# Optimization experiments

Hardware: AMD Instinct MI355X
Metric: run time of the kernel (lower is better)

Reference implementation:

```python
import jax, jax.numpy as jnp
import numpy as np

# Adaptive softmax config (PyTorch AdaptiveLogSoftmaxWithLoss defaults, div_value=4)
N_CLASSES = 50000
CUTOFFS = (2000, 10000)          # shortlist size 2000; clusters [2000,10000), [10000,50000)
SHORTLIST = CUTOFFS[0]
HEAD_SIZE = SHORTLIST + 2        # shortlist + one logit per cluster
IN_FEAT = 512                    # output_size of MLP == in_features of adaptive softmax
HSZ0, HSZ1 = 128, 32             # in_features // 4**(i+1)
C0 = CUTOFFS[1] - CUTOFFS[0]     # 8000
C1 = N_CLASSES - CUTOFFS[1]      # 40000


def setup_inputs() -> dict:
    key = jax.random.key(0)
    ks = jax.random.split(key, 16)
    s = 0.02
    inp = {
        "x": jax.random.normal(ks[0], (4096, 512), jnp.float32),
        "t": jax.random.randint(ks[1], (4096,), 0, N_CLASSES, jnp.int64),
        # MLP params: 512 -> 2048 -> 128 -> 512, ReLU after each
        "W1": jax.random.normal(ks[2], (2048, 512), jnp.float32) * s,
        "b1": jnp.zeros((2048,), jnp.float32),
        "W2": jax.random.normal(ks[3], (128, 2048), jnp.float32) * s,
        "b2": jnp.zeros((128,), jnp.float32),
        "W3": jax.random.normal(ks[4], (512, 128), jnp.float32) * s,
        "b3": jnp.zeros((512,), jnp.float32),
        # adaptive softmax head: shortlist + 2 cluster logits
        "head_W": jax.random.normal(ks[5], (HEAD_SIZE, IN_FEAT), jnp.float32) * s,
        "head_b": jnp.zeros((HEAD_SIZE,), jnp.float32),
        # tail cluster 0: 512 -> 128 -> 8000 (no bias, no activation)
        "t0a": jax.random.normal(ks[6], (HSZ0, IN_FEAT), jnp.float32) * s,
        "t0b": jax.random.normal(ks[7], (C0, HSZ0), jnp.float32) * s,
        # tail cluster 1: 512 -> 32 -> 40000
        "t1a": jax.random.normal(ks[8], (HSZ1, IN_FEAT), jnp.float32) * s,
        "t1b": jax.random.normal(ks[9], (C1, HSZ1), jnp.float32) * s,
    }
    return inp


def _mlp(x, W1, b1, W2, b2, W3, b3):
    h = jax.nn.relu(x @ W1.T + b1)
    h = jax.nn.relu(h @ W2.T + b2)
    return jax.nn.relu(h @ W3.T + b3)   # [N, 512]


def _adaptive_log_softmax(score, t, head_W, head_b, t0a, t0b, t1a, t1b):
    n = score.shape[0]
    rows = jnp.arange(n)
    head_lsm = jax.nn.log_softmax(score @ head_W.T + head_b, axis=-1)   # [N, 2002]
    # tail clusters: two low-rank projections then log-softmax over cluster classes
    tail0_lsm = jax.nn.log_softmax((score @ t0a.T) @ t0b.T, axis=-1)    # [N, 8000]
    tail1_lsm = jax.nn.log_softmax((score @ t1a.T) @ t1b.T, axis=-1)    # [N, 40000]

    lp_short = head_lsm[rows, jnp.clip(t, 0, SHORTLIST - 1)]
    lp_c0 = head_lsm[:, SHORTLIST] + tail0_lsm[rows, jnp.clip(t - CUTOFFS[0], 0, C0 - 1)]
    lp_c1 = head_lsm[:, SHORTLIST + 1] + tail1_lsm[rows, jnp.clip(t - CUTOFFS[1], 0, C1 - 1)]

    out = jnp.where(t < CUTOFFS[0], lp_short, jnp.where(t < CUTOFFS[1], lp_c0, lp_c1))  # [N]
    loss = -jnp.mean(out)
    return out, loss


def reference(x, t, W1, b1, W2, b2, W3, b3, head_W, head_b, t0a, t0b, t1a, t1b):
    score = _mlp(x, W1, b1, W2, b2, W3, b3)
    out, loss = _adaptive_log_softmax(score, t, head_W, head_b, t0a, t0b, t1a, t1b)
    return out, loss
```

## Files before the change

kernel.cpp:

```cpp
#include <hip/hip_runtime.h>
#include <math.h>

typedef __attribute__((ext_vector_type(8))) short bf16x8;
typedef __attribute__((ext_vector_type(4))) float f32x4;

#define NROWS 4096
#define SHORTLIST 2000
#define HEADC 2002
#define CUT1 10000
#define C0_CLS 8000
#define C1_CLS 40000
#define L2E 1.4426950408889634f
#define LN2 0.6931471805599453f

#define NH_P  16
#define NC0_P 25
#define NC1_P 125

__device__ __forceinline__ float fexp2(float x) {
#if __has_builtin(__builtin_amdgcn_exp2f)
  return __builtin_amdgcn_exp2f(x);
#else
  return exp2f(x);
#endif
}

__device__ __forceinline__ unsigned short f2b(float f) {
  unsigned u = __float_as_uint(f);
  unsigned r = (u + 0x7FFFu + ((u >> 16) & 1u)) >> 16;
  return (unsigned short)r;
}
__device__ __forceinline__ float b2f(unsigned short u) {
  return __uint_as_float(((unsigned)u) << 16);
}

__global__ __launch_bounds__(256) void cvt_all(
    const float* __restrict__ s0, unsigned short* __restrict__ d0,
    const float* __restrict__ s1, unsigned short* __restrict__ d1,
    const float* __restrict__ s2, unsigned short* __restrict__ d2,
    const float* __restrict__ s3, unsigned short* __restrict__ d3,
    const float* __restrict__ s4, unsigned short* __restrict__ d4,
    const float* __restrict__ s5, unsigned short* __restrict__ d5,
    const float* __restrict__ s6, unsigned short* __restrict__ d6,
    const float* __restrict__ s7, unsigned short* __restrict__ d7,
    const float* __restrict__ s8, unsigned short* __restrict__ d8)
{
  const float* src; unsigned short* dst; int n4;
  switch (blockIdx.y) {
    case 0: src = s0; dst = d0; n4 = 4096 * 512 / 4;   break;
    case 1: src = s1; dst = d1; n4 = 2048 * 512 / 4;   break;
    case 2: src = s2; dst = d2; n4 = 128 * 2048 / 4;   break;
    case 3: src = s3; dst = d3; n4 = 512 * 128 / 4;    break;
    case 4: src = s4; dst = d4; n4 = HEADC * 512 / 4;  break;
    case 5: src = s5; dst = d5; n4 = 128 * 512 / 4;    break;
    case 6: src = s6; dst = d6; n4 = 8000 * 128 / 4;   break;
    case 7: src = s7; dst = d7; n4 = 32 * 512 / 4;     break;
    default: src = s8; dst = d8; n4 = 40000 * 32 / 4;  break;
  }
  for (int i = blockIdx.x * 256 + threadIdx.x; i < n4; i += 256 * gridDim.x) {
    float4 v = ((const float4*)src)[i];
    ushort4 o;
    o.x = f2b(v.x); o.y = f2b(v.y); o.z = f2b(v.z); o.w = f2b(v.w);
    ((ushort4*)dst)[i] = o;
  }
}

template<bool BIAS, bool RELU, bool F32OUT>
__global__ __launch_bounds__(256) void gemm_lds(
    const unsigned short* __restrict__ A, const unsigned short* __restrict__ W,
    const float* __restrict__ bias, void* __restrict__ outp,
    int M, int N, int lda, int Kseg)
{
  __shared__ __align__(16) unsigned short As[128 * 32];
  __shared__ __align__(16) unsigned short Bs[128 * 32];

  const int tid  = threadIdx.x;
  const int lane = tid & 63;
  const int wv   = tid >> 6;
  const int cl   = lane & 15;
  const int ko   = lane >> 4;
  const int wr   = (wv >> 1) * 64;
  const int wc   = (wv & 1) * 64;
  const int row0 = blockIdx.y * 128;
  const int col0 = blockIdx.x * 128;
  const int koff = blockIdx.z * Kseg;

  const int sr0 = tid >> 2;
  const int ssl = tid & 3;

  f32x4 acc[4][4];
#pragma unroll
  for (int p = 0; p < 4; ++p)
#pragma unroll
    for (int q = 0; q < 4; ++q) acc[p][q] = (f32x4){0.f, 0.f, 0.f, 0.f};

  const unsigned short* aSrc = A + (size_t)(row0 + sr0) * lda + koff + ssl * 8;
  const unsigned short* bSrc = W + (size_t)(col0 + sr0) * lda + koff + ssl * 8;
  const size_t half = (size_t)64 * lda;

  bf16x8 sa0 = *(const bf16x8*)(aSrc);
  bf16x8 sa1 = *(const bf16x8*)(aSrc + half);
  bf16x8 sb0 = *(const bf16x8*)(bSrc);
  bf16x8 sb1 = *(const bf16x8*)(bSrc + half);

  const int nK = Kseg / 32;
  for (int ks = 0; ks < nK; ++ks) {
    __syncthreads();
    *(bf16x8*)&As[(size_t)sr0 * 32 + ssl * 8]        = sa0;
    *(bf16x8*)&As[(size_t)(sr0 + 64) * 32 + ssl * 8] = sa1;
    *(bf16x8*)&Bs[(size_t)sr0 * 32 + ssl * 8]        = sb0;
    *(bf16x8*)&Bs[(size_t)(sr0 + 64) * 32 + ssl * 8] = sb1;
    __syncthreads();
    if (ks + 1 < nK) {
      const int k1 = (ks + 1) * 32;
      sa0 = *(const bf16x8*)(aSrc + k1);
      sa1 = *(const bf16x8*)(aSrc + k1 + half);
      sb0 = *(const bf16x8*)(bSrc + k1);
      sb1 = *(const bf16x8*)(bSrc + k1 + half);
    }
    bf16x8 aF[4], bF[4];
#pragma unroll
    for (int p = 0; p < 4; ++p)
      aF[p] = *(const bf16x8*)&As[(size_t)(wr + p * 16 + cl) * 32 + ko * 8];
#pragma unroll
    for (int q = 0; q < 4; ++q)
      bF[q] = *(const bf16x8*)&Bs[(size_t)(wc + q * 16 + cl) * 32 + ko * 8];
#pragma unroll
    for (int p = 0; p < 4; ++p)
#pragma unroll
      for (int q = 0; q < 4; ++q)
        acc[p][q] = __builtin_amdgcn_mfma_f32_16x16x32_bf16(aF[p], bF[q], acc[p][q], 0, 0, 0);
  }

  if constexpr (F32OUT) {
    float* P = (float*)outp + (size_t)blockIdx.z * M * N;
#pragma unroll
    for (int q = 0; q < 4; ++q) {
      const int col = col0 + wc + q * 16 + cl;
#pragma unroll
      for (int p = 0; p < 4; ++p)
#pragma unroll
        for (int j = 0; j < 4; ++j) {
          const int R = row0 + wr + p * 16 + 4 * ko + j;
          P[(size_t)R * N + col] = acc[p][q][j];
        }
    }
  } else {
    unsigned short* C = (unsigned short*)outp;
#pragma unroll
    for (int q = 0; q < 4; ++q) {
      const int col = col0 + wc + q * 16 + cl;
      float bs = 0.f;
      if (BIAS) bs = bias[col];
#pragma unroll
      for (int p = 0; p < 4; ++p)
#pragma unroll
        for (int j = 0; j < 4; ++j) {
          const int R = row0 + wr + p * 16 + 4 * ko + j;
          float v = acc[p][q][j] + bs;
          if (RELU) v = fmaxf(v, 0.f);
          C[(size_t)R * N + col] = f2b(v);
        }
    }
  }
}

template<int SK, bool BIAS, bool RELU>
__global__ __launch_bounds__(256) void splitk_reduce(
    const float* __restrict__ P, const float* __restrict__ bias,
    unsigned short* __restrict__ out, int MN4, int N)
{
  const int i = blockIdx.x * 256 + threadIdx.x;
  if (i >= MN4) return;
  float4 v = ((const float4*)P)[i];
#pragma unroll
  for (int z = 1; z < SK; ++z) {
    float4 p = ((const float4*)(P + (size_t)z * MN4 * 4))[i];
    v.x += p.x; v.y += p.y; v.z += p.z; v.w += p.w;
  }
  if (BIAS) {
    const int col = (i % (N / 4)) * 4;
    float4 b = *(const float4*)(bias + col);
    v.x += b.x; v.y += b.y; v.z += b.z; v.w += b.w;
  }
  if (RELU) {
    v.x = fmaxf(v.x, 0.f); v.y = fmaxf(v.y, 0.f);
    v.z = fmaxf(v.z, 0.f); v.w = fmaxf(v.w, 0.f);
  }
  ushort4 o;
  o.x = f2b(v.x); o.y = f2b(v.y); o.z = f2b(v.z); o.w = f2b(v.w);
  ((ushort4*)out)[i] = o;
}

__global__ __launch_bounds__(256) void head_gemm_lse(
    const unsigned short* __restrict__ A,
    const unsigned short* __restrict__ W,
    const float* __restrict__ bias,
    float* __restrict__ pm, float* __restrict__ ps)
{
  __shared__ __align__(16) unsigned short As[128 * 32];
  __shared__ __align__(16) unsigned short Bs[128 * 32];
  __shared__ float lm[4][64], ls[4][64];

  const int lda  = 512;
  const int tid  = threadIdx.x;
  const int lane = tid & 63;
  const int wv   = tid >> 6;
  const int cl   = lane & 15;
  const int ko   = lane >> 4;
  const int wr   = (wv >> 1) * 64;
  const int wc   = (wv & 1) * 64;
  const int row0 = blockIdx.y * 128;
  const int col0 = blockIdx.x * 128;

  const int sr0 = tid >> 2;
  const int ssl = tid & 3;

  f32x4 acc[4][4];
#pragma unroll
  for (int p = 0; p < 4; ++p)
#pragma unroll
    for (int q = 0; q < 4; ++q) acc[p][q] = (f32x4){0.f, 0.f, 0.f, 0.f};

  const unsigned short* aSrc = A + (size_t)(row0 + sr0) * lda + ssl * 8;
  const unsigned short* bSrc0 = W + (size_t)min(col0 + sr0, HEADC - 1) * lda + ssl * 8;
  const unsigned short* bSrc1 = W + (size_t)min(col0 + sr0 + 64, HEADC - 1) * lda + ssl * 8;
  const size_t half = (size_t)64 * lda;

  bf16x8 sa0 = *(const bf16x8*)(aSrc);
  bf16x8 sa1 = *(const bf16x8*)(aSrc + half);
  bf16x8 sb0 = *(const bf16x8*)(bSrc0);
  bf16x8 sb1 = *(const bf16x8*)(bSrc1);

  const int nK = 512 / 32;
  for (int ks = 0; ks < nK; ++ks) {
    __syncthreads();
    *(bf16x8*)&As[(size_t)sr0 * 32 + ssl * 8]        = sa0;
    *(bf16x8*)&As[(size_t)(sr0 + 64) * 32 + ssl * 8] = sa1;
    *(bf16x8*)&Bs[(size_t)sr0 * 32 + ssl * 8]        = sb0;
    *(bf16x8*)&Bs[(size_t)(sr0 + 64) * 32 + ssl * 8] = sb1;
    __syncthreads();
    if (ks + 1 < nK) {
      const int k1 = (ks + 1) * 32;
      sa0 = *(const bf16x8*)(aSrc + k1);
      sa1 = *(const bf16x8*)(aSrc + k1 + half);
      sb0 = *(const bf16x8*)(bSrc0 + k1);
      sb1 = *(const bf16x8*)(bSrc1 + k1);
    }
    bf16x8 aF[4], bF[4];
#pragma unroll
    for (int p = 0; p < 4; ++p)
      aF[p] = *(const bf16x8*)&As[(size_t)(wr + p * 16 + cl) * 32 + ko * 8];
#pragma unroll
    for (int q = 0; q < 4; ++q)
      bF[q] = *(const bf16x8*)&Bs[(size_t)(wc + q * 16 + cl) * 32 + ko * 8];
#pragma unroll
    for (int p = 0; p < 4; ++p)
#pragma unroll
      for (int q = 0; q < 4; ++q)
        acc[p][q] = __builtin_amdgcn_mfma_f32_16x16x32_bf16(aF[p], bF[q], acc[p][q], 0, 0, 0);
  }

  float bl2[4]; int colq[4];
#pragma unroll
  for (int q = 0; q < 4; ++q) {
    colq[q] = col0 + wc + q * 16 + cl;
    bl2[q] = bias[min(colq[q], HEADC - 1)] * L2E;
  }

  float mr[4][4], sr_[4][4];
#pragma unroll
  for (int p = 0; p < 4; ++p)
#pragma unroll
    for (int j = 0; j < 4; ++j) {
      float vv[4], mm = -3e38f;
#pragma unroll
      for (int q = 0; q < 4; ++q) {
        float v = fmaf(acc[p][q][j], L2E, bl2[q]);
        if (colq[q] >= HEADC) v = -1e30f;
        vv[q] = v;
        mm = fmaxf(mm, v);
      }
      float ss = 0.f;
#pragma unroll
      for (int q = 0; q < 4; ++q) ss += fexp2(vv[q] - mm);
      mr[p][j] = mm;
      sr_[p][j] = ss;
    }

#pragma unroll
  for (int mask = 1; mask <= 8; mask <<= 1) {
#pragma unroll
    for (int p = 0; p < 4; ++p)
#pragma unroll
      for (int j = 0; j < 4; ++j) {
        const float mo = __shfl_xor(mr[p][j], mask);
        const float so = __shfl_xor(sr_[p][j], mask);
        const float mn = fmaxf(mr[p][j], mo);
        sr_[p][j] = sr_[p][j] * fexp2(mr[p][j] - mn) + so * fexp2(mo - mn);
        mr[p][j] = mn;
      }
  }

  if (cl == 0) {
#pragma unroll
    for (int p = 0; p < 4; ++p)
#pragma unroll
      for (int j = 0; j < 4; ++j) {
        lm[wv][p * 16 + 4 * ko + j] = mr[p][j];
        ls[wv][p * 16 + 4 * ko + j] = sr_[p][j];
      }
  }
  __syncthreads();
  if (tid < 128) {
    const int pair = tid >> 6, idx = tid & 63;
    const float m0 = lm[pair * 2][idx], m1 = lm[pair * 2 + 1][idx];
    const float M = fmaxf(m0, m1);
    const float S = ls[pair * 2][idx] * fexp2(m0 - M) + ls[pair * 2 + 1][idx] * fexp2(m1 - M);
    const int grow = row0 + tid;
    pm[(size_t)blockIdx.x * NROWS + grow] = M;
    ps[(size_t)blockIdx.x * NROWS + grow] = S;
  }
}

template<int WR, int WC, bool BIAS, bool RELU>
__global__ __launch_bounds__(256) void gemm_mfma(
    const unsigned short* __restrict__ A, const unsigned short* __restrict__ W,
    const float* __restrict__ bias, unsigned short* __restrict__ C,
    int M, int N, int K)
{
  const int lane = threadIdx.x & 63;
  const int wv   = threadIdx.x >> 6;
  const int cl   = lane & 15;
  const int ko   = lane >> 4;
  const int rw   = (blockIdx.y * WR + (wv / WC)) * 64;
  const int cw   = (blockIdx.x * WC + (wv % WC)) * 32;

  f32x4 acc[4][2];
#pragma unroll
  for (int p = 0; p < 4; ++p)
#pragma unroll
    for (int q = 0; q < 2; ++q) acc[p][q] = (f32x4){0.f, 0.f, 0.f, 0.f};

  const unsigned short* ap = A + (size_t)(rw + cl) * K + ko * 8;
  const unsigned short* bp = W + (size_t)(cw + cl) * K + ko * 8;
  const size_t rstep = (size_t)16 * K;

#pragma unroll 2
  for (int kb = 0; kb < K; kb += 32) {
    bf16x8 a[4], b[2];
#pragma unroll
    for (int p = 0; p < 4; ++p) a[p] = *(const bf16x8*)(ap + p * rstep + kb);
#pragma unroll
    for (int q = 0; q < 2; ++q) b[q] = *(const bf16x8*)(bp + q * rstep + kb);
#pragma unroll
    for (int p = 0; p < 4; ++p)
#pragma unroll
      for (int q = 0; q < 2; ++q)
        acc[p][q] = __builtin_amdgcn_mfma_f32_16x16x32_bf16(a[p], b[q], acc[p][q], 0, 0, 0);
  }

#pragma unroll
  for (int q = 0; q < 2; ++q) {
    const int col = cw + q * 16 + cl;
    if (col >= N) continue;
    float bs = 0.f;
    if (BIAS) bs = bias[col];
#pragma unroll
    for (int p = 0; p < 4; ++p) {
#pragma unroll
      for (int j = 0; j < 4; ++j) {
        const int R = rw + p * 16 + 4 * ko + j;
        float v = acc[p][q][j] + bs;
        if (RELU) v = fmaxf(v, 0.f);
        C[(size_t)R * N + col] = f2b(v);
      }
    }
  }
}

template<int KBLK, int ROWT, int U, int NIT>
__global__ __launch_bounds__(256) void fused_lse_tail(
    const unsigned short* __restrict__ H,
    const unsigned short* __restrict__ W,
    int NCB,
    float* __restrict__ pm, float* __restrict__ ps)
{
  const int K    = KBLK * 32;
  const int lane = threadIdx.x & 63;
  const int wv   = threadIdx.x >> 6;
  const int cl   = lane & 15;
  const int ko   = lane >> 4;
  const int r0   = blockIdx.x * (64 * ROWT) + wv * (16 * ROWT);

  bf16x8 aF[ROWT][KBLK];
#pragma unroll
  for (int rt = 0; rt < ROWT; ++rt) {
    const unsigned short* ap = H + (size_t)(r0 + rt * 16 + cl) * K + ko * 8;
#pragma unroll
    for (int kk = 0; kk < KBLK; ++kk) aF[rt][kk] = *(const bf16x8*)(ap + kk * 32);
  }

  float m[ROWT][4], s[ROWT][4];
#pragma unroll
  for (int rt = 0; rt < ROWT; ++rt)
#pragma unroll
    for (int j = 0; j < 4; ++j) { m[rt][j] = -1e30f; s[rt][j] = 0.f; }

  const unsigned short* wbase =
      W + (size_t)(blockIdx.y * (U * NIT) * 16 + cl) * K + ko * 8;
  const size_t chunkstep = (size_t)16 * K;

  bf16x8 bA[U][KBLK], bB[U][KBLK];

  auto loadB = [&](bf16x8 (&bf)[U][KBLK], int it) {
    const unsigned short* p = wbase + (size_t)it * U * chunkstep;
#pragma unroll
    for (int u = 0; u < U; ++u)
#pragma unroll
      for (int kk = 0; kk < KBLK; ++kk)
        bf[u][kk] = *(const bf16x8*)(p + u * chunkstep + kk * 32);
  };

  auto consume = [&](bf16x8 (&bf)[U][KBLK]) {
    f32x4 acc[ROWT][U];
#pragma unroll
    for (int rt = 0; rt < ROWT; ++rt)
#pragma unroll
      for (int u = 0; u < U; ++u) acc[rt][u] = (f32x4){0.f, 0.f, 0.f, 0.f};
#pragma unroll
    for (int kk = 0; kk < KBLK; ++kk)
#pragma unroll
      for (int u = 0; u < U; ++u)
#pragma unroll
        for (int rt = 0; rt < ROWT; ++rt)
          acc[rt][u] = __builtin_amdgcn_mfma_f32_16x16x32_bf16(aF[rt][kk], bf[u][kk], acc[rt][u], 0, 0, 0);

    float nm[ROWT][4];
#pragma unroll
    for (int rt = 0; rt < ROWT; ++rt)
#pragma unroll
      for (int j = 0; j < 4; ++j) nm[rt][j] = m[rt][j];
#pragma unroll
    for (int rt = 0; rt < ROWT; ++rt)
#pragma unroll
      for (int u = 0; u < U; ++u)
#pragma unroll
        for (int j = 0; j < 4; ++j)
          nm[rt][j] = fmaxf(nm[rt][j], acc[rt][u][j] * L2E);

    float dd = -3e38f;
#pragma unroll
    for (int rt = 0; rt < ROWT; ++rt)
#pragma unroll
      for (int j = 0; j < 4; ++j) dd = fmaxf(dd, nm[rt][j] - m[rt][j]);

    if (__any(dd > 8.f)) {
#pragma unroll
      for (int rt = 0; rt < ROWT; ++rt)
#pragma unroll
        for (int j = 0; j < 4; ++j) {
          s[rt][j] *= fexp2(m[rt][j] - nm[rt][j]);
          m[rt][j] = nm[rt][j];
        }
    }
#pragma unroll
    for (int rt = 0; rt < ROWT; ++rt)
#pragma unroll
      for (int u = 0; u < U; ++u)
#pragma unroll
        for (int j = 0; j < 4; ++j)
          s[rt][j] += fexp2(fmaf(acc[rt][u][j], L2E, -m[rt][j]));
  };

  loadB(bA, 0);
#pragma unroll
  for (int it = 0; it < NIT; it += 2) {
    loadB(bB, it + 1);
    consume(bA);
    if (it + 2 < NIT) loadB(bA, it + 2);
    consume(bB);
  }

#pragma unroll
  for (int mask = 1; mask <= 8; mask <<= 1) {
#pragma unroll
    for (int rt = 0; rt < ROWT; ++rt)
#pragma unroll
      for (int j = 0; j < 4; ++j) {
        const float mo = __shfl_xor(m[rt][j], mask);
        const float so = __shfl_xor(s[rt][j], mask);
        const float mn = fmaxf(m[rt][j], mo);
        s[rt][j] = s[rt][j] * fexp2(m[rt][j] - mn) + so * fexp2(mo - mn);
        m[rt][j] = mn;
      }
  }
  if (cl == 0) {
#pragma unroll
    for (int rt = 0; rt < ROWT; ++rt)
#pragma unroll
      for (int j = 0; j < 4; ++j) {
        const int R = r0 + rt * 16 + 4 * ko + j;
        pm[(size_t)blockIdx.y * NROWS + R] = m[rt][j];
        ps[(size_t)blockIdx.y * NROWS + R] = s[rt][j];
      }
  }
}

__global__ __launch_bounds__(256) void gather_kernel(
    const unsigned short* __restrict__ Sb,
    const unsigned short* __restrict__ hWb,
    const float* __restrict__ head_b,
    const unsigned short* __restrict__ h0b,
    const unsigned short* __restrict__ t0bb,
    const unsigned short* __restrict__ h1b,
    const unsigned short* __restrict__ t1bb,
    const int* __restrict__ t,
    float* __restrict__ gsh, float* __restrict__ gc0, float* __restrict__ gc1,
    float* __restrict__ tg0, float* __restrict__ tg1)
{
  const int lane = threadIdx.x & 63;
  const int row  = blockIdx.x * 4 + (threadIdx.x >> 6);
  const int tv   = t[row];
  const int ch   = min(max(tv, 0), SHORTLIST - 1);
  const int c0   = min(max(tv - SHORTLIST, 0), C0_CLS - 1);
  const int c1   = min(max(tv - CUT1, 0), C1_CLS - 1);

  float acc[5] = {0.f, 0.f, 0.f, 0.f, 0.f};

  {
    bf16x8 sv = *(const bf16x8*)(Sb + (size_t)row * 512 + lane * 8);
    bf16x8 w0 = *(const bf16x8*)(hWb + (size_t)ch * 512 + lane * 8);
    bf16x8 w1 = *(const bf16x8*)(hWb + (size_t)SHORTLIST * 512 + lane * 8);
    bf16x8 w2 = *(const bf16x8*)(hWb + (size_t)(SHORTLIST + 1) * 512 + lane * 8);
#pragma unroll
    for (int e = 0; e < 8; ++e) {
      const float sf = b2f((unsigned short)sv[e]);
      acc[0] = fmaf(sf, b2f((unsigned short)w0[e]), acc[0]);
      acc[1] = fmaf(sf, b2f((unsigned short)w1[e]), acc[1]);
      acc[2] = fmaf(sf, b2f((unsigned short)w2[e]), acc[2]);
    }
  }
  if (lane < 16) {
    bf16x8 hv = *(const bf16x8*)(h0b + (size_t)row * 128 + lane * 8);
    bf16x8 wv = *(const bf16x8*)(t0bb + (size_t)c0 * 128 + lane * 8);
#pragma unroll
    for (int e = 0; e < 8; ++e)
      acc[3] = fmaf(b2f((unsigned short)hv[e]), b2f((unsigned short)wv[e]), acc[3]);
  }
  if (lane < 4) {
    bf16x8 hv = *(const bf16x8*)(h1b + (size_t)row * 32 + lane * 8);
    bf16x8 wv = *(const bf16x8*)(t1bb + (size_t)c1 * 32 + lane * 8);
#pragma unroll
    for (int e = 0; e < 8; ++e)
      acc[4] = fmaf(b2f((unsigned short)hv[e]), b2f((unsigned short)wv[e]), acc[4]);
  }

#pragma unroll
  for (int mask = 1; mask < 64; mask <<= 1)
#pragma unroll
    for (int k = 0; k < 5; ++k) acc[k] += __shfl_xor(acc[k], mask);

  if (lane == 0) {
    gsh[row] = acc[0] + head_b[ch];
    gc0[row] = acc[1] + head_b[SHORTLIST];
    gc1[row] = acc[2] + head_b[SHORTLIST + 1];
    tg0[row] = acc[3];
    tg1[row] = acc[4];
  }
}

__global__ __launch_bounds__(256) void combine_kernel(
    const int* __restrict__ t,
    const float* __restrict__ pmh, const float* __restrict__ psh,
    const float* __restrict__ gsh, const float* __restrict__ gc0,
    const float* __restrict__ gc1,
    const float* __restrict__ pm0, const float* __restrict__ ps0,
    const float* __restrict__ tg0,
    const float* __restrict__ pm1, const float* __restrict__ ps1,
    const float* __restrict__ tg1,
    float* __restrict__ out)
{
  const int r = blockIdx.x * 256 + threadIdx.x;
  if (r >= NROWS) return;

  float M = -1e30f, S = 0.f;
  for (int c = 0; c < NH_P; ++c) M = fmaxf(M, pmh[c * NROWS + r]);
  for (int c = 0; c < NH_P; ++c) S += psh[c * NROWS + r] * fexp2(pmh[c * NROWS + r] - M);
  const float hl = (M + log2f(S)) * LN2;

  const int tv = t[r];
  float o;
  if (tv < SHORTLIST) {
    o = gsh[r] - hl;
  } else if (tv < CUT1) {
    float M0 = -1e30f, S0 = 0.f;
    for (int c = 0; c < NC0_P; ++c) M0 = fmaxf(M0, pm0[c * NROWS + r]);
    for (int c = 0; c < NC0_P; ++c) S0 += ps0[c * NROWS + r] * fexp2(pm0[c * NROWS + r] - M0);
    o = (gc0[r] - hl) + (tg0[r] - (M0 + log2f(S0)) * LN2);
  } else {
    float M1 = -1e30f, S1 = 0.f;
    for (int c = 0; c < NC1_P; ++c) M1 = fmaxf(M1, pm1[c * NROWS + r]);
    for (int c = 0; c < NC1_P; ++c) S1 += ps1[c * NROWS + r] * fexp2(pm1[c * NROWS + r] - M1);
    o = (gc1[r] - hl) + (tg1[r] - (M1 + log2f(S1)) * LN2);
  }
  out[r] = o;
}

__global__ __launch_bounds__(256) void loss_kernel(
    const float* __restrict__ out, float* __restrict__ loss)
{
  __shared__ float sred[256];
  const int tid = threadIdx.x;
  float s = 0.f;
  for (int i = tid; i < NROWS; i += 256) s += out[i];
  sred[tid] = s;
  __syncthreads();
  for (int st = 128; st > 0; st >>= 1) {
    if (tid < st) sred[tid] += sred[tid + st];
    __syncthreads();
  }
  if (tid == 0) *loss = -sred[0] / (float)NROWS;
}

extern "C" void kernel_launch(void* const* d_in, const int* in_sizes, int n_in,
                              void* d_out, int out_size, void* d_ws, size_t ws_size,
                              hipStream_t stream)
{
  const float* x      = (const float*)d_in[0];
  const int*   t      = (const int*)  d_in[1];
  const float* W1     = (const float*)d_in[2];
  const float* b1     = (const float*)d_in[3];
  const float* W2     = (const float*)d_in[4];
  const float* b2     = (const float*)d_in[5];
  const float* W3     = (const float*)d_in[6];
  const float* b3     = (const float*)d_in[7];
  const float* head_W = (const float*)d_in[8];
  const float* head_b = (const float*)d_in[9];
  const float* t0a    = (const float*)d_in[10];
  const float* t0b    = (const float*)d_in[11];
  const float* t1a    = (const float*)d_in[12];
  const float* t1b    = (const float*)d_in[13];

  unsigned short* p16 = (unsigned short*)d_ws;
  unsigned short* xb  = p16; p16 += 4096ull * 512;
  unsigned short* W1b = p16; p16 += 2048ull * 512;
  unsigned short* W2b = p16; p16 += 128ull  * 2048;
  unsigned short* W3b = p16; p16 += 512ull  * 128;
  unsigned short* hWb = p16; p16 += (size_t)HEADC * 512;
  unsigned short* t0ab= p16; p16 += 128ull  * 512;
  unsigned short* t0bb= p16; p16 += 8000ull * 128;
  unsigned short* t1ab= p16; p16 += 32ull   * 512;
  unsigned short* t1bb= p16; p16 += 40000ull* 32;
  unsigned short* H1b = p16; p16 += 4096ull * 2048;
  unsigned short* H2b = p16; p16 += 4096ull * 128;
  unsigned short* Sb  = p16; p16 += 4096ull * 512;
  unsigned short* h0b = p16; p16 += 4096ull * 128;
  unsigned short* h1b = p16; p16 += 4096ull * 32;

  float* pf  = (float*)p16;
  float* pmh = pf; pf += 4096 * NH_P;
  float* psh = pf; pf += 4096 * NH_P;
  float* pm0 = pf; pf += 4096 * NC0_P;
  float* ps0 = pf; pf += 4096 * NC0_P;
  float* pm1 = pf; pf += 4096 * NC1_P;
  float* ps1 = pf; pf += 4096 * NC1_P;
  float* gsh = pf; pf += 4096;
  float* gc0 = pf; pf += 4096;
  float* gc1 = pf; pf += 4096;
  float* tg0 = pf; pf += 4096;
  float* tg1 = pf; pf += 4096;
  float* Pbuf = pf; pf += 4ull * 4096 * 128;

  float* out = (float*)d_out;

  const dim3 blk(256);

  cvt_all<<<dim3(256, 9), blk, 0, stream>>>(
      x, xb, W1, W1b, W2, W2b, W3, W3b, head_W, hWb,
      t0a, t0ab, t0b, t0bb, t1a, t1ab, t1b, t1bb);

  gemm_lds<true, true, false><<<dim3(16, 32), blk, 0, stream>>>(
      xb, W1b, b1, H1b, 4096, 2048, 512, 512);
  gemm_lds<false, false, true><<<dim3(1, 32, 4), blk, 0, stream>>>(
      H1b, W2b, nullptr, Pbuf, 4096, 128, 2048, 512);
  splitk_reduce<4, true, true><<<dim3(512), blk, 0, stream>>>(
      Pbuf, b2, H2b, 4096 * 128 / 4, 128);
  gemm_lds<true, true, false><<<dim3(4, 32), blk, 0, stream>>>(
      H2b, W3b, b3, Sb, 4096, 512, 128, 128);

  gemm_lds<false, false, true><<<dim3(1, 32, 4), blk, 0, stream>>>(
      Sb, t0ab, nullptr, Pbuf, 4096, 128, 512, 128);
  splitk_reduce<4, false, false><<<dim3(512), blk, 0, stream>>>(
      Pbuf, nullptr, h0b, 4096 * 128 / 4, 128);
  gemm_mfma<4, 1, false, false><<<dim3(1, 16), blk, 0, stream>>>(
      Sb, t1ab, nullptr, h1b, 4096, 32, 512);

  head_gemm_lse<<<dim3(16, 32), blk, 0, stream>>>(Sb, hWb, head_b, pmh, psh);

  fused_lse_tail<4, 2, 2, 10><<<dim3(32, NC0_P), blk, 0, stream>>>(h0b, t0bb, NC0_P, pm0, ps0);
  fused_lse_tail<1, 2, 5, 4 ><<<dim3(32, NC1_P), blk, 0, stream>>>(h1b, t1bb, NC1_P, pm1, ps1);

  gather_kernel<<<dim3(NROWS / 4), blk, 0, stream>>>(
      Sb, hWb, head_b, h0b, t0bb, h1b, t1bb, t, gsh, gc0, gc1, tg0, tg1);

  combine_kernel<<<dim3((NROWS + 255) / 256), blk, 0, stream>>>(
      t, pmh, psh, gsh, gc0, gc1, pm0, ps0, tg0, pm1, ps1, tg1, out);
  loss_kernel<<<dim3(1), blk, 0, stream>>>(out, out + NROWS);
}
```

Before: 301.1 us.

## Pre-scale score by log2e, swizzle blocks across XCDs, split tail exp accumulators

The final MLP layer now multiplies its output by log2(e) before rounding to bf16. All downstream logits are therefore already in base-2 units, which removes the per-element L2E multiply in the head and tail LSE kernels. Head bias in the gather step and the final ln2 conversion in the combine step are adjusted to match. GEMM and head kernels also remap block indices so neighbouring tiles land on the same XCD for L2 reuse, and the tail LSE splits its exp sum into two accumulators to shorten the dependency chain. Rescaling before the bf16 rounding slightly changes the numerics.

```diff
diff --git a/kernel.cpp b/kernel.cpp
--- a/kernel.cpp
+++ b/kernel.cpp
@@ -32,6 +32,15 @@
 }
 __device__ __forceinline__ float b2f(unsigned short u) {
   return __uint_as_float(((unsigned)u) << 16);
+}
+
+__device__ __forceinline__ void xcd_swz(int& bx, int& by) {
+  const int gx = gridDim.x;
+  const int nwg = gx * gridDim.y;
+  const int orig = by * gx + bx;
+  const int wg = (orig & 7) * (nwg >> 3) + (orig >> 3);
+  bx = wg % gx;
+  by = wg / gx;
 }
 
 __global__ __launch_bounds__(256) void cvt_all(
@@ -65,7 +74,7 @@
   }
 }
 
-template<bool BIAS, bool RELU, bool F32OUT>
+template<bool BIAS, bool RELU, bool F32OUT, bool SCL>
 __global__ __launch_bounds__(256) void gemm_lds(
     const unsigned short* __restrict__ A, const unsigned short* __restrict__ W,
     const float* __restrict__ bias, void* __restrict__ outp,
@@ -73,6 +82,9 @@
 {
   __shared__ __align__(16) unsigned short As[128 * 32];
   __shared__ __align__(16) unsigned short Bs[128 * 32];
+
+  int bx = blockIdx.x, by = blockIdx.y;
+  xcd_swz(bx, by);
 
   const int tid  = threadIdx.x;
   const int lane = tid & 63;
@@ -81,8 +93,8 @@
   const int ko   = lane >> 4;
   const int wr   = (wv >> 1) * 64;
   const int wc   = (wv & 1) * 64;
-  const int row0 = blockIdx.y * 128;
-  const int col0 = blockIdx.x * 128;
+  const int row0 = by * 128;
+  const int col0 = bx * 128;
   const int koff = blockIdx.z * Kseg;
 
   const int sr0 = tid >> 2;
@@ -159,6 +171,7 @@
           const int R = row0 + wr + p * 16 + 4 * ko + j;
           float v = acc[p][q][j] + bs;
           if (RELU) v = fmaxf(v, 0.f);
+          if (SCL)  v *= L2E;
           C[(size_t)R * N + col] = f2b(v);
         }
     }
@@ -201,6 +214,9 @@
   __shared__ __align__(16) unsigned short As[128 * 32];
   __shared__ __align__(16) unsigned short Bs[128 * 32];
   __shared__ float lm[4][64], ls[4][64];
+
+  int bx = blockIdx.x, by = blockIdx.y;
+  xcd_swz(bx, by);
 
   const int lda  = 512;
   const int tid  = threadIdx.x;
@@ -210,8 +226,8 @@
   const int ko   = lane >> 4;
   const int wr   = (wv >> 1) * 64;
   const int wc   = (wv & 1) * 64;
-  const int row0 = blockIdx.y * 128;
-  const int col0 = blockIdx.x * 128;
+  const int row0 = by * 128;
+  const int col0 = bx * 128;
 
   const int sr0 = tid >> 2;
   const int ssl = tid & 3;
@@ -273,14 +289,14 @@
   for (int p = 0; p < 4; ++p)
 #pragma unroll
     for (int j = 0; j < 4; ++j) {
-      float vv[4], mm = -3e38f;
+      float vv[4];
 #pragma unroll
       for (int q = 0; q < 4; ++q) {
-        float v = fmaf(acc[p][q][j], L2E, bl2[q]);
+        float v = acc[p][q][j] + bl2[q];
         if (colq[q] >= HEADC) v = -1e30f;
         vv[q] = v;
-        mm = fmaxf(mm, v);
       }
+      const float mm = fmaxf(fmaxf(vv[0], vv[1]), fmaxf(vv[2], vv[3]));
       float ss = 0.f;
 #pragma unroll
       for (int q = 0; q < 4; ++q) ss += fexp2(vv[q] - mm);
@@ -318,8 +334,8 @@
     const float M = fmaxf(m0, m1);
     const float S = ls[pair * 2][idx] * fexp2(m0 - M) + ls[pair * 2 + 1][idx] * fexp2(m1 - M);
     const int grow = row0 + tid;
-    pm[(size_t)blockIdx.x * NROWS + grow] = M;
-    ps[(size_t)blockIdx.x * NROWS + grow] = S;
+    pm[(size_t)bx * NROWS + grow] = M;
+    ps[(size_t)bx * NROWS + grow] = S;
   }
 }
 
@@ -401,11 +417,11 @@
     for (int kk = 0; kk < KBLK; ++kk) aF[rt][kk] = *(const bf16x8*)(ap + kk * 32);
   }
 
-  float m[ROWT][4], s[ROWT][4];
+  float m[ROWT][4], s[ROWT][4], s2[ROWT][4];
 #pragma unroll
   for (int rt = 0; rt < ROWT; ++rt)
 #pragma unroll
-    for (int j = 0; j < 4; ++j) { m[rt][j] = -1e30f; s[rt][j] = 0.f; }
+    for (int j = 0; j < 4; ++j) { m[rt][j] = -1e30f; s[rt][j] = 0.f; s2[rt][j] = 0.f; }
 
   const unsigned short* wbase =
       W + (size_t)(blockIdx.y * (U * NIT) * 16 + cl) * K + ko * 8;
@@ -436,32 +452,32 @@
         for (int rt = 0; rt < ROWT; ++rt)
           acc[rt][u] = __builtin_amdgcn_mfma_f32_16x16x32_bf16(aF[rt][kk], bf[u][kk], acc[rt][u], 0, 0, 0);
 
-    float nm[ROWT][4];
+    float cm[ROWT][4];
 #pragma unroll
     for (int rt = 0; rt < ROWT; ++rt)
 #pragma unroll
-      for (int j = 0; j < 4; ++j) nm[rt][j] = m[rt][j];
+      for (int j = 0; j < 4; ++j) {
+        float c = acc[rt][0][j];
+#pragma unroll
+        for (int u = 1; u < U; ++u) c = fmaxf(c, acc[rt][u][j]);
+        cm[rt][j] = c;
+      }
+
+    float dd = -3e38f;
 #pragma unroll
     for (int rt = 0; rt < ROWT; ++rt)
 #pragma unroll
-      for (int u = 0; u < U; ++u)
-#pragma unroll
-        for (int j = 0; j < 4; ++j)
-          nm[rt][j] = fmaxf(nm[rt][j], acc[rt][u][j] * L2E);
-
-    float dd = -3e38f;
-#pragma unroll
-    for (int rt = 0; rt < ROWT; ++rt)
-#pragma unroll
-      for (int j = 0; j < 4; ++j) dd = fmaxf(dd, nm[rt][j] - m[rt][j]);
+      for (int j = 0; j < 4; ++j) dd = fmaxf(dd, cm[rt][j] - m[rt][j]);
 
     if (__any(dd > 8.f)) {
 #pragma unroll
       for (int rt = 0; rt < ROWT; ++rt)
 #pragma unroll
         for (int j = 0; j < 4; ++j) {
-          s[rt][j] *= fexp2(m[rt][j] - nm[rt][j]);
-          m[rt][j] = nm[rt][j];
+          const float mn = fmaxf(m[rt][j], cm[rt][j]);
+          const float sc = fexp2(m[rt][j] - mn);
+          s[rt][j] *= sc; s2[rt][j] *= sc;
+          m[rt][j] = mn;
         }
     }
 #pragma unroll
@@ -469,8 +485,10 @@
 #pragma unroll
       for (int u = 0; u < U; ++u)
 #pragma unroll
-        for (int j = 0; j < 4; ++j)
-          s[rt][j] += fexp2(fmaf(acc[rt][u][j], L2E, -m[rt][j]));
+        for (int j = 0; j < 4; ++j) {
+          const float e = fexp2(acc[rt][u][j] - m[rt][j]);
+          if (u & 1) s2[rt][j] += e; else s[rt][j] += e;
+        }
   };
 
   loadB(bA, 0);
@@ -481,6 +499,11 @@
     if (it + 2 < NIT) loadB(bA, it + 2);
     consume(bB);
   }
+
+#pragma unroll
+  for (int rt = 0; rt < ROWT; ++rt)
+#pragma unroll
+    for (int j = 0; j < 4; ++j) s[rt][j] += s2[rt][j];
 
 #pragma unroll
   for (int mask = 1; mask <= 8; mask <<= 1) {
@@ -562,9 +585,9 @@
     for (int k = 0; k < 5; ++k) acc[k] += __shfl_xor(acc[k], mask);
 
   if (lane == 0) {
-    gsh[row] = acc[0] + head_b[ch];
-    gc0[row] = acc[1] + head_b[SHORTLIST];
-    gc1[row] = acc[2] + head_b[SHORTLIST + 1];
+    gsh[row] = acc[0] + head_b[ch] * L2E;
+    gc0[row] = acc[1] + head_b[SHORTLIST] * L2E;
+    gc1[row] = acc[2] + head_b[SHORTLIST + 1] * L2E;
     tg0[row] = acc[3];
     tg1[row] = acc[4];
   }
@@ -587,24 +610,24 @@
   float M = -1e30f, S = 0.f;
   for (int c = 0; c < NH_P; ++c) M = fmaxf(M, pmh[c * NROWS + r]);
   for (int c = 0; c < NH_P; ++c) S += psh[c * NROWS + r] * fexp2(pmh[c * NROWS + r] - M);
-  const float hl = (M + log2f(S)) * LN2;
+  const float hl2 = M + log2f(S);
 
   const int tv = t[r];
-  float o;
+  float o2;
   if (tv < SHORTLIST) {
-    o = gsh[r] - hl;
+    o2 = gsh[r] - hl2;
   } else if (tv < CUT1) {
     float M0 = -1e30f, S0 = 0.f;
     for (int c = 0; c < NC0_P; ++c) M0 = fmaxf(M0, pm0[c * NROWS + r]);
     for (int c = 0; c < NC0_P; ++c) S0 += ps0[c * NROWS + r] * fexp2(pm0[c * NROWS + r] - M0);
-    o = (gc0[r] - hl) + (tg0[r] - (M0 + log2f(S0)) * LN2);
+    o2 = (gc0[r] - hl2) + (tg0[r] - (M0 + log2f(S0)));
   } else {
     float M1 = -1e30f, S1 = 0.f;
     for (int c = 0; c < NC1_P; ++c) M1 = fmaxf(M1, pm1[c * NROWS + r]);
     for (int c = 0; c < NC1_P; ++c) S1 += ps1[c * NROWS + r] * fexp2(pm1[c * NROWS + r] - M1);
-    o = (gc1[r] - hl) + (tg1[r] - (M1 + log2f(S1)) * LN2);
-  }
-  out[r] = o;
+    o2 = (gc1[r] - hl2) + (tg1[r] - (M1 + log2f(S1)));
+  }
+  out[r] = o2 * LN2;
 }
 
 __global__ __launch_bounds__(256) void loss_kernel(
@@ -680,16 +703,16 @@
       x, xb, W1, W1b, W2, W2b, W3, W3b, head_W, hWb,
       t0a, t0ab, t0b, t0bb, t1a, t1ab, t1b, t1bb);
 
-  gemm_lds<true, true, false><<<dim3(16, 32), blk, 0, stream>>>(
+  gemm_lds<true, true, false, false><<<dim3(16, 32), blk, 0, stream>>>(
       xb, W1b, b1, H1b, 4096, 2048, 512, 512);
-  gemm_lds<false, false, true><<<dim3(1, 32, 4), blk, 0, stream>>>(
+  gemm_lds<false, false, true, false><<<dim3(1, 32, 4), blk, 0, stream>>>(
       H1b, W2b, nullptr, Pbuf, 4096, 128, 2048, 512);
   splitk_reduce<4, true, true><<<dim3(512), blk, 0, stream>>>(
       Pbuf, b2, H2b, 4096 * 128 / 4, 128);
-  gemm_lds<true, true, false><<<dim3(4, 32), blk, 0, stream>>>(
+  gemm_lds<true, true, false, true><<<dim3(4, 32), blk, 0, stream>>>(
       H2b, W3b, b3, Sb, 4096, 512, 128, 128);
 
-  gemm_lds<false, false, true><<<dim3(1, 32, 4), blk, 0, stream>>>(
+  gemm_lds<false, false, true, false><<<dim3(1, 32, 4), blk, 0, stream>>>(
       Sb, t0ab, nullptr, Pbuf, 4096, 128, 512, 128);
   splitk_reduce<4, false, false><<<dim3(512), blk, 0, stream>>>(
       Pbuf, nullptr, h0b, 4096 * 128 / 4, 128);
```

After: 294.5 us. -2.2%, faster.
